# Performance work log

Hardware: AMD Instinct MI355X
Metric: run time of the kernel (lower is better)

Reference implementation:

```python
import jax, jax.numpy as jnp
import numpy as np

B, N = 2, 131072          # batch, expanded node slots (divisible by flag_size)
FEAT = 69                 # org(3) + pos(3) + uids(63)
KERNELS = 128
FLAG_SIZE = 4             # 1 << dims, dims = 2
BINS = 16                 # 1 << flag_size


def _conv1d(x, w, b, stride=1, padding='SAME'):
    # keras Conv1D: x [B,N,Cin], w [K,Cin,Cout], relu activation
    y = jax.lax.conv_general_dilated(x, w, (stride,), padding,
                                     dimension_numbers=('NWC', 'WIO', 'NWC'))
    return jax.nn.relu(y + b)


def setup_inputs() -> dict:
    key = jax.random.key(0)
    ks = jax.random.split(key, 12)

    def g(k, shape):
        fan_in = int(np.prod(shape[:-1]))
        return (jax.random.normal(k, shape, jnp.float32) / np.sqrt(fan_in)).astype(jnp.float32)

    c_x = FEAT + KERNELS                 # 197 after each pre conv concat
    c_flags = 2 * FEAT + KERNELS         # 266 flags-head input
    c_sym = c_flags + FLAG_SIZE          # 270 symbols-branch input

    return {
        'inputs': jax.random.normal(ks[0], (B, N, FEAT), jnp.float32),
        'w_pre0': g(ks[1], (3, FEAT, KERNELS)),   'b_pre0': jnp.zeros((KERNELS,), jnp.float32),
        'w_pre1': g(ks[2], (3, c_x, KERNELS)),    'b_pre1': jnp.zeros((KERNELS,), jnp.float32),
        'w_flags': g(ks[3], (c_flags, FLAG_SIZE)), 'b_flags': jnp.zeros((FLAG_SIZE,), jnp.float32),
        'w_merge': g(ks[4], (FLAG_SIZE, c_sym, KERNELS)), 'b_merge': jnp.zeros((KERNELS,), jnp.float32),
        'w_post0': g(ks[5], (3, KERNELS, KERNELS)), 'b_post0': jnp.zeros((KERNELS,), jnp.float32),
        'w_post1': g(ks[6], (3, KERNELS, KERNELS)), 'b_post1': jnp.zeros((KERNELS,), jnp.float32),
        'w_post2': g(ks[7], (3, KERNELS, KERNELS)), 'b_post2': jnp.zeros((KERNELS,), jnp.float32),
        'w_post3': g(ks[8], (3, KERNELS, KERNELS)), 'b_post3': jnp.zeros((KERNELS,), jnp.float32),
        'w_sym': g(ks[9], (KERNELS, BINS)),        'b_sym': jnp.zeros((BINS,), jnp.float32),
    }


def _forward(inputs, w_pre0, b_pre0, w_pre1, b_pre1, w_flags, b_flags,
             w_merge, b_merge, w_post0, b_post0, w_post1, b_post1,
             w_post2, b_post2, w_post3, b_post3, w_sym, b_sym):
    # pos offsets = (3, 6); pos = inputs[..., 3:5] (2 columns)
    pos = inputs[..., 3:5]
    sort = jnp.argsort(pos, axis=-2)                       # [B, N, 2]
    # gather with batch_dims=1 along node axis
    X = jnp.take_along_axis(inputs, sort[..., 1:2], axis=1)   # sorted by pos col 1
    x0 = jax.lax.stop_gradient(X)                            # [B, N, 69]
    X = jnp.concatenate([x0, _conv1d(X, w_pre0, b_pre0)], axis=-1)  # [B, N, 197]
    X = jnp.concatenate([x0, _conv1d(X, w_pre1, b_pre1)], axis=-1)  # [B, N, 197]
    X = jnp.concatenate([X, jnp.take_along_axis(inputs, sort[..., 0:1], axis=1)], axis=-1)  # [B, N, 266]

    F = jax.nn.sigmoid(X @ w_flags + b_flags)               # [B, N, 4]

    S = jax.lax.stop_gradient(jnp.concatenate([F, X], axis=-1))     # [B, N, 270]
    S = _conv1d(S, w_merge, b_merge, stride=FLAG_SIZE, padding='VALID')  # [B, N/4, 128]
    for w, b in ((w_post0, b_post0), (w_post1, b_post1), (w_post2, b_post2), (w_post3, b_post3)):
        S = _conv1d(S, w, b)
    S = jax.nn.softmax(S @ w_sym + b_sym, axis=-1)          # [B, N/4, 16]

    Fd = (F[..., 0] - F[..., 1]).reshape(F.shape[0], -1, FLAG_SIZE)  # [B, N/4, 4]
    return jnp.concatenate([Fd, S], axis=-1)                # [B, N/4, 20]


def reference(inputs, w_pre0, b_pre0, w_pre1, b_pre1, w_flags, b_flags,
              w_merge, b_merge, w_post0, b_post0, w_post1, b_post1,
              w_post2, b_post2, w_post3, b_post3, w_sym, b_sym):
    return _forward(inputs, w_pre0, b_pre0, w_pre1, b_pre1, w_flags, b_flags,
                    w_merge, b_merge, w_post0, b_post0, w_post1, b_post1,
                    w_post2, b_post2, w_post3, b_post3, w_sym, b_sym)
```

## Files before the change

kernel.cpp:

```cpp
#include <hip/hip_runtime.h>
#include <hip/hip_bf16.h>
#include <math.h>

#define NPOS 131072
#define NF   69
#define NMRG 32768
#define TILE 2048
#define TPS  64
#define NSORT 4

typedef __attribute__((ext_vector_type(8))) short short8;
typedef __bf16 bf16x8 __attribute__((ext_vector_type(8)));
typedef __attribute__((ext_vector_type(4))) float f32x4;

static __device__ inline bf16x8 as_bf16x8(short8 v){ union{short8 s; bf16x8 b;} u; u.s=v; return u.b; }
static __device__ inline short f2bf(float x){ __hip_bfloat16 h = __float2bfloat16(x); return *(short*)&h; }
static __device__ inline float bf2f(short s){ return __uint_as_float(((unsigned)(unsigned short)s)<<16); }

static __device__ inline void gld16(const short* g, short* l){
  __builtin_amdgcn_global_load_lds(
      (const __attribute__((address_space(1))) unsigned int*)g,
      (__attribute__((address_space(3))) unsigned int*)l, 16, 0, 0);
}

__global__ void k_make_keys(const float* __restrict__ inp, unsigned* __restrict__ kA,
                            unsigned* __restrict__ vA){
  unsigned t = blockIdx.x*256u + threadIdx.x;
  unsigned s = t >> 17, i = t & (NPOS-1u);
  unsigned b = s >> 1, ch = 3u + (s & 1u);
  float x = inp[((size_t)b*NPOS + i)*NF + ch];
  unsigned u = __float_as_uint(x);
  u = (u & 0x80000000u) ? ~u : (u | 0x80000000u);
  kA[t] = u; vA[t] = i;
}

__global__ __launch_bounds__(256) void k_hist(const unsigned* __restrict__ src,
                                              unsigned* __restrict__ hist, int shift){
  __shared__ unsigned h[256];
  int tid = threadIdx.x;
  h[tid] = 0u; __syncthreads();
  int s = blockIdx.x / TPS, tile = blockIdx.x % TPS;
  const unsigned* ks = src + (size_t)s*NPOS + (size_t)tile*TILE;
  for (int r = 0; r < TILE/256; ++r){
    unsigned d = (ks[r*256 + tid] >> shift) & 255u;
    atomicAdd(&h[d], 1u);
  }
  __syncthreads();
  hist[s*16384 + tid*TPS + tile] = h[tid];
}

__global__ __launch_bounds__(256) void k_scan(unsigned* __restrict__ hist){
  __shared__ unsigned tot[256];
  int tid = threadIdx.x; int s = blockIdx.x;
  unsigned* g = hist + s*16384;
  unsigned sum = 0;
  for (int q = 0; q < 64; ++q) sum += g[tid*64 + q];
  tot[tid] = sum;
  __syncthreads();
  if (tid == 0){
    unsigned run = 0;
    for (int t = 0; t < 256; ++t){ unsigned tmp = tot[t]; tot[t] = run; run += tmp; }
  }
  __syncthreads();
  unsigned run = tot[tid];
  for (int q = 0; q < 64; ++q){ unsigned tmp = g[tid*64+q]; g[tid*64+q] = run; run += tmp; }
}

#define EPT 16
__global__ __launch_bounds__(128) void k_scatter(const unsigned* __restrict__ srcK,
    const unsigned* __restrict__ srcV, unsigned* __restrict__ dstK, unsigned* __restrict__ dstV,
    const unsigned* __restrict__ off, int shift){
  __shared__ unsigned short cnt[256*128];
  int tid = threadIdx.x;
  unsigned* cz = (unsigned*)cnt;
  for (int idx = tid; idx < 256*128/2; idx += 128) cz[idx] = 0u;
  __syncthreads();
  int s = blockIdx.x / TPS, tile = blockIdx.x % TPS;
  const unsigned* ks = srcK + (size_t)s*NPOS + (size_t)tile*TILE;
  const unsigned* vs = srcV + (size_t)s*NPOS + (size_t)tile*TILE;
  unsigned k8[EPT], v8[EPT];
  #pragma unroll
  for (int r = 0; r < EPT; ++r){
    k8[r] = ks[tid*EPT + r];
    v8[r] = vs[tid*EPT + r];
    unsigned d = (k8[r] >> shift) & 255u;
    cnt[d*128 + tid]++;
  }
  __syncthreads();
  for (int dd = 0; dd < 2; ++dd){
    int d = tid + dd*128;
    unsigned run = 0;
    for (int t = 0; t < 128; ++t){ unsigned tmp = cnt[d*128 + t]; cnt[d*128 + t] = (unsigned short)run; run += tmp; }
  }
  __syncthreads();
  const unsigned* ob = off + s*16384;
  #pragma unroll
  for (int r = 0; r < EPT; ++r){
    unsigned d = (k8[r] >> shift) & 255u;
    unsigned rk = cnt[d*128 + tid];
    cnt[d*128 + tid] = (unsigned short)(rk + 1u);
    unsigned pos = ob[d*TPS + tile] + rk;
    dstK[(size_t)s*NPOS + pos] = k8[r];
    dstV[(size_t)s*NPOS + pos] = v8[r];
  }
}

__global__ __launch_bounds__(256) void k_gath(const float* __restrict__ inp,
    const unsigned* __restrict__ P1, const unsigned* __restrict__ P0,
    short* __restrict__ XA, short* __restrict__ Xcat, int b){
  int t = blockIdx.x*256 + threadIdx.x;
  int i = t >> 7, c = t & 127;
  if (c < 69){
    short s1 = f2bf(inp[((size_t)b*NPOS + P1[i])*NF + c]);
    XA[(size_t)i*224 + 128 + c] = s1;
    Xcat[(size_t)i*272 + 132 + c] = s1;
    Xcat[(size_t)i*272 + 201 + c] = f2bf(inp[((size_t)b*NPOS + P0[i])*NF + c]);
  } else if (c == 69){
    Xcat[(size_t)i*272 + 270] = 0;
    Xcat[(size_t)i*272 + 271] = 0;
  }
}

__global__ void k_prepB(const float* __restrict__ w, short* __restrict__ out,
                        int KC, int NQ, int mode, int total){
  int t = blockIdx.x*256 + threadIdx.x;
  if (t >= total) return;
  int lane = t & 63, ni = (t>>6) & 1, ksub = (t>>7) & 1;
  int rest = t >> 8;
  int q = rest % NQ;
  int wv = rest / NQ;
  int tap = q / KC, cc = q - tap*KC;
  int nn = wv*32 + ni*16 + (lane & 15);
  int chb = cc*64 + ksub*32 + ((lane >> 4) & 3)*8;
  short o[8];
  #pragma unroll
  for (int e = 0; e < 8; ++e){
    int ch = chb + e;
    float val = 0.f;
    if (mode == 0){ if (ch < 69)  val = w[((size_t)tap*69  + ch)*128 + nn]; }
    else if (mode == 1){
      if (ch < 128)      val = w[((size_t)tap*197 + 69 + ch)*128 + nn];
      else if (ch < 197) val = w[((size_t)tap*197 + ch - 128)*128 + nn];
    }
    else if (mode == 2){ if (ch < 128) val = w[((size_t)tap*128 + ch)*128 + nn]; }
    else {
      int tm = ch / 272, cm = ch - tm*272;
      int orig = -1;
      if (cm < 128)      orig = 73 + cm;
      else if (cm < 201) orig = cm - 128;
      else if (cm < 270) orig = cm;
      if (orig >= 0) val = w[((size_t)tm*270 + orig)*128 + nn];
    }
    o[e] = f2bf(val);
  }
  *(short8*)(out + (size_t)t*8) = *(short8*)o;
}

__global__ void k_prepWf(const float* __restrict__ wf, float* __restrict__ out){
  int t = blockIdx.x*256 + threadIdx.x;
  if (t >= 1088) return;
  int c = t >> 2, q = t & 3;
  float v = 0.f;
  if (c < 128)                 v = wf[(69 + c)*4 + q];
  else if (c >= 132 && c < 201) v = wf[(c - 132)*4 + q];
  else if (c >= 201 && c < 270) v = wf[(197 + c - 201)*4 + q];
  out[t] = v;
}

#define OSTR 132

template<int CPAD>
__global__ __launch_bounds__(256) void k_conv3r(
    const short* __restrict__ src, int sstride, int coff, int cin,
    const short* __restrict__ wB, const float* __restrict__ bias,
    short* __restrict__ dst, int dstride, int n)
{
  constexpr int KC = CPAD/64;
  constexpr int NSTEP = 3*KC;
  constexpr int ASTR = CPAD + 8;
  constexpr int AG = CPAD/8;
  constexpr size_t ABYTES = (size_t)66*ASTR*2;
  constexpr size_t OBYTES = (size_t)64*OSTR*4;
  constexpr size_t LBYTES = (ABYTES > OBYTES) ? ABYTES : OBYTES;
  __shared__ __attribute__((aligned(16))) char LDS[LBYTES];
  short* A_s = (short*)LDS;
  float* OT  = (float*)LDS;
  int tid = threadIdx.x;
  int i0 = blockIdx.x*64;
  int wv = tid >> 6, lane = tid & 63;
  int lm = lane & 15, lk = lane >> 4;

  for (int idx = tid; idx < 66*AG; idx += 256){
    int r = idx / AG, g = idx - r*AG;
    int pos = i0 - 1 + r;
    short8 v = {0,0,0,0,0,0,0,0};
    if (pos >= 0 && pos < n && g*8 < cin){
      const short* sp = src + (size_t)pos*sstride + coff + g*8;
      if (g*8 + 8 <= cin) v = *(const short8*)sp;
      else { for (int j = 0; g*8 + j < cin; ++j) v[j] = sp[j]; }
    }
    *(short8*)(A_s + r*ASTR + g*8) = v;
  }
  __syncthreads();

  const short* wBw = wB + (size_t)wv*NSTEP*2048 + (size_t)lane*8;
  f32x4 acc[4][2] = {};
  #pragma unroll
  for (int tp = 0; tp < 3; ++tp){
    bf16x8 bfr[KC][2][2];
    #pragma unroll
    for (int c = 0; c < KC; ++c)
      #pragma unroll
      for (int ksub = 0; ksub < 2; ++ksub)
        #pragma unroll
        for (int ni = 0; ni < 2; ++ni)
          bfr[c][ksub][ni] = as_bf16x8(*(const short8*)(
              wBw + (((size_t)(tp*KC + c)*2 + ksub)*2 + ni)*512));
    #pragma unroll
    for (int c = 0; c < KC; ++c){
      #pragma unroll
      for (int ksub = 0; ksub < 2; ++ksub){
        bf16x8 a[4];
        #pragma unroll
        for (int mi = 0; mi < 4; ++mi)
          a[mi] = as_bf16x8(*(const short8*)(A_s + (mi*16+lm+tp)*ASTR + c*64 + ksub*32 + lk*8));
        #pragma unroll
        for (int mi = 0; mi < 4; ++mi)
          #pragma unroll
          for (int ni = 0; ni < 2; ++ni)
            acc[mi][ni] = __builtin_amdgcn_mfma_f32_16x16x32_bf16(a[mi], bfr[c][ksub][ni], acc[mi][ni], 0, 0, 0);
      }
    }
  }
  __syncthreads();
  float b0 = bias[wv*32 + lm], b1 = bias[wv*32 + 16 + lm];
  #pragma unroll
  for (int mi = 0; mi < 4; ++mi)
    #pragma unroll
    for (int ni = 0; ni < 2; ++ni){
      float bb = ni ? b1 : b0;
      #pragma unroll
      for (int r = 0; r < 4; ++r)
        OT[(mi*16 + lk*4 + r)*OSTR + wv*32 + ni*16 + lm] = fmaxf(acc[mi][ni][r] + bb, 0.f);
    }
  __syncthreads();
  {
    int r = tid >> 2, q = tid & 3;
    const float* row = OT + r*OSTR + q*32;
    short o[32];
    #pragma unroll
    for (int jc = 0; jc < 8; ++jc){
      f32x4 v = *(const f32x4*)(row + jc*4);
      #pragma unroll
      for (int e = 0; e < 4; ++e) o[jc*4+e] = f2bf(v[e]);
    }
    short* dp = dst + (size_t)(i0 + r)*dstride + q*32;
    #pragma unroll
    for (int v8 = 0; v8 < 4; ++v8) *(short8*)(dp + v8*8) = *(short8*)(o + v8*8);
  }
}

__global__ __launch_bounds__(256) void k_mergem3(const short* __restrict__ Xf,
    const short* __restrict__ wB, const float* __restrict__ bias, short* __restrict__ dst)
{
  constexpr size_t OBYTES = (size_t)64*OSTR*4;
  __shared__ __attribute__((aligned(16))) char LDS[OBYTES];
  short* A_s = (short*)LDS;
  float* OT  = (float*)LDS;
  int tid = threadIdx.x;
  int j0 = blockIdx.x*64;
  int wv = tid >> 6, lane = tid & 63;
  int lm = lane & 15, lk = lane >> 4;
  auto stageA = [&](int s){
    #pragma unroll
    for (int it = 0; it < 2; ++it){
      int slot = it*256 + tid;
      int r = slot >> 3, kv = slot & 7;
      const short* gp = Xf + (size_t)(j0 + r)*1088 + s*64 + ((kv ^ (r&7))*8);
      gld16(gp, A_s + (s&1)*4096 + slot*8);
    }
  };
  const short* wBl = wB + (size_t)wv*17*2048 + (size_t)lane*8;
  auto LB = [&](int s, int ks, int ni){
    return as_bf16x8(*(const short8*)(wBl + ((size_t)(s*2 + ks)*2 + ni)*512));
  };
  bf16x8 c00 = LB(0,0,0), c01 = LB(0,0,1), c10 = LB(0,1,0), c11 = LB(0,1,1);
  stageA(0);
  __syncthreads();
  f32x4 acc[4][2] = {};
  for (int s = 0; s < 17; ++s){
    bf16x8 n00, n01, n10, n11;
    if (s < 16){
      n00 = LB(s+1,0,0); n01 = LB(s+1,0,1); n10 = LB(s+1,1,0); n11 = LB(s+1,1,1);
      stageA(s+1);
    }
    const short* Ab = A_s + (s&1)*4096;
    bf16x8 a[4];
    #pragma unroll
    for (int mi = 0; mi < 4; ++mi){
      int r = mi*16 + lm;
      a[mi] = as_bf16x8(*(const short8*)(Ab + r*64 + ((lk ^ (r&7))*8)));
    }
    #pragma unroll
    for (int mi = 0; mi < 4; ++mi){
      acc[mi][0] = __builtin_amdgcn_mfma_f32_16x16x32_bf16(a[mi], c00, acc[mi][0], 0, 0, 0);
      acc[mi][1] = __builtin_amdgcn_mfma_f32_16x16x32_bf16(a[mi], c01, acc[mi][1], 0, 0, 0);
    }
    #pragma unroll
    for (int mi = 0; mi < 4; ++mi){
      int r = mi*16 + lm;
      a[mi] = as_bf16x8(*(const short8*)(Ab + r*64 + (((4+lk) ^ (r&7))*8)));
    }
    #pragma unroll
    for (int mi = 0; mi < 4; ++mi){
      acc[mi][0] = __builtin_amdgcn_mfma_f32_16x16x32_bf16(a[mi], c10, acc[mi][0], 0, 0, 0);
      acc[mi][1] = __builtin_amdgcn_mfma_f32_16x16x32_bf16(a[mi], c11, acc[mi][1], 0, 0, 0);
    }
    __syncthreads();
    c00 = n00; c01 = n01; c10 = n10; c11 = n11;
  }
  float b0 = bias[wv*32 + lm], b1 = bias[wv*32 + 16 + lm];
  #pragma unroll
  for (int mi = 0; mi < 4; ++mi)
    #pragma unroll
    for (int ni = 0; ni < 2; ++ni){
      float bb = ni ? b1 : b0;
      #pragma unroll
      for (int r = 0; r < 4; ++r)
        OT[(mi*16 + lk*4 + r)*OSTR + wv*32 + ni*16 + lm] = fmaxf(acc[mi][ni][r] + bb, 0.f);
    }
  __syncthreads();
  {
    int r = tid >> 2, q = tid & 3;
    const float* row = OT + r*OSTR + q*32;
    short o[32];
    #pragma unroll
    for (int jc = 0; jc < 8; ++jc){
      f32x4 v = *(const f32x4*)(row + jc*4);
      #pragma unroll
      for (int e = 0; e < 4; ++e) o[jc*4+e] = f2bf(v[e]);
    }
    short* dp = dst + (size_t)(j0 + r)*128 + q*32;
    #pragma unroll
    for (int v8 = 0; v8 < 4; ++v8) *(short8*)(dp + v8*8) = *(short8*)(o + v8*8);
  }
}

__global__ __launch_bounds__(256) void k_flags2(short* __restrict__ Xcat,
    const float* __restrict__ Wf2, const float* __restrict__ bf, float* __restrict__ F){
  size_t i = (size_t)blockIdx.x*256 + threadIdx.x;
  const short* x = Xcat + i*272;
  float a0 = bf[0], a1 = bf[1], a2 = bf[2], a3 = bf[3];
  for (int g = 0; g < 34; ++g){
    short8 x8 = *(const short8*)(x + g*8);
    #pragma unroll
    for (int e = 0; e < 8; ++e){
      float xv = bf2f(x8[e]);
      const float* w = Wf2 + (g*8+e)*4;
      a0 = fmaf(xv,w[0],a0); a1 = fmaf(xv,w[1],a1); a2 = fmaf(xv,w[2],a2); a3 = fmaf(xv,w[3],a3);
    }
  }
  float f0 = 1.f/(1.f+expf(-a0)), f1 = 1.f/(1.f+expf(-a1));
  float f2 = 1.f/(1.f+expf(-a2)), f3 = 1.f/(1.f+expf(-a3));
  float* f = F + i*4;
  f[0]=f0; f[1]=f1; f[2]=f2; f[3]=f3;
  short* xc = Xcat + i*272 + 128;
  xc[0]=f2bf(f0); xc[1]=f2bf(f1); xc[2]=f2bf(f2); xc[3]=f2bf(f3);
}

__global__ __launch_bounds__(256) void k_out(const short* __restrict__ S,
    const float* __restrict__ F, const float* __restrict__ Ws, const float* __restrict__ bs,
    float* __restrict__ out, int b){
  size_t j = (size_t)blockIdx.x*256 + threadIdx.x;
  float l[16];
  #pragma unroll
  for (int t = 0; t < 16; ++t) l[t] = bs[t];
  const short* s = S + j*128;
  for (int g = 0; g < 16; ++g){
    short8 x8 = *(const short8*)(s + g*8);
    #pragma unroll
    for (int e = 0; e < 8; ++e){
      float x = bf2f(x8[e]);
      const float* w = Ws + (g*8+e)*16;
      #pragma unroll
      for (int t = 0; t < 16; ++t) l[t] = fmaf(x, w[t], l[t]);
    }
  }
  float m = l[0];
  #pragma unroll
  for (int t = 1; t < 16; ++t) m = fmaxf(m, l[t]);
  float sum = 0.f;
  #pragma unroll
  for (int t = 0; t < 16; ++t){ l[t] = expf(l[t]-m); sum += l[t]; }
  float inv = 1.f/sum;
  float* o = out + ((size_t)b*NMRG + j)*20;
  #pragma unroll
  for (int k = 0; k < 4; ++k){
    size_t r = (size_t)(4*j + k)*4;
    o[k] = F[r] - F[r+1];
  }
  #pragma unroll
  for (int t = 0; t < 16; ++t) o[4+t] = l[t]*inv;
}

extern "C" void kernel_launch(void* const* d_in, const int* in_sizes, int n_in,
                              void* d_out, int out_size, void* d_ws, size_t ws_size,
                              hipStream_t stream){
  const float* inp     = (const float*)d_in[0];
  const float* w_pre0  = (const float*)d_in[1];
  const float* b_pre0  = (const float*)d_in[2];
  const float* w_pre1  = (const float*)d_in[3];
  const float* b_pre1  = (const float*)d_in[4];
  const float* w_flags = (const float*)d_in[5];
  const float* b_flags = (const float*)d_in[6];
  const float* w_merge = (const float*)d_in[7];
  const float* b_merge = (const float*)d_in[8];
  const float* w_post[4] = {(const float*)d_in[9], (const float*)d_in[11],
                            (const float*)d_in[13], (const float*)d_in[15]};
  const float* b_post[4] = {(const float*)d_in[10], (const float*)d_in[12],
                            (const float*)d_in[14], (const float*)d_in[16]};
  const float* w_sym   = (const float*)d_in[17];
  const float* b_sym   = (const float*)d_in[18];
  float* outp = (float*)d_out;

  char* p = (char*)d_ws;
  unsigned* kA = (unsigned*)p; p += (size_t)NSORT*NPOS*4;
  unsigned* vA = (unsigned*)p; p += (size_t)NSORT*NPOS*4;
  unsigned* kB = (unsigned*)p; p += (size_t)NSORT*NPOS*4;
  unsigned* vB = (unsigned*)p; p += (size_t)NSORT*NPOS*4;
  unsigned* hist = (unsigned*)p; p += (size_t)NSORT*16384*4;
  short* XA   = (short*)p; p += (size_t)NPOS*224*2;
  short* Xcat = (short*)p; p += (size_t)NPOS*272*2;
  float* Fbuf = (float*)p; p += (size_t)NPOS*4*4;
  short* M0   = (short*)p; p += (size_t)NMRG*128*2;
  short* M1   = (short*)p; p += (size_t)NMRG*128*2;
  short* wb0  = (short*)p; p += (size_t)3*2*8192*2;
  short* wb1  = (short*)p; p += (size_t)3*4*8192*2;
  short* wbq0 = (short*)p; p += (size_t)3*2*8192*2;
  short* wbq1 = (short*)p; p += (size_t)3*2*8192*2;
  short* wbq2 = (short*)p; p += (size_t)3*2*8192*2;
  short* wbq3 = (short*)p; p += (size_t)3*2*8192*2;
  short* wbm  = (short*)p; p += (size_t)17*8192*2;
  float* wf2  = (float*)p; p += (size_t)272*4*4;
  if ((size_t)(p - (char*)d_ws) > ws_size) return;
  short* wbq[4] = {wbq0, wbq1, wbq2, wbq3};

  k_prepB<<<(6144 +255)/256, 256, 0, stream>>>(w_pre0, wb0, 2, 6, 0, 6144);
  k_prepB<<<(12288+255)/256, 256, 0, stream>>>(w_pre1, wb1, 4, 12, 1, 12288);
  for (int i = 0; i < 4; ++i)
    k_prepB<<<(6144+255)/256, 256, 0, stream>>>(w_post[i], wbq[i], 2, 6, 2, 6144);
  k_prepB<<<(17408+255)/256, 256, 0, stream>>>(w_merge, wbm, 17, 17, 3, 17408);
  k_prepWf<<<5, 256, 0, stream>>>(w_flags, wf2);

  k_make_keys<<<NSORT*NPOS/256, 256, 0, stream>>>(inp, kA, vA);
  unsigned *sk = kA, *sv = vA, *dk = kB, *dv = vB;
  for (int pass = 0; pass < 4; ++pass){
    int shift = pass*8;
    k_hist<<<NSORT*TPS, 256, 0, stream>>>(sk, hist, shift);
    k_scan<<<NSORT, 256, 0, stream>>>(hist);
    k_scatter<<<NSORT*TPS, 128, 0, stream>>>(sk, sv, dk, dv, hist, shift);
    unsigned* t;
    t = sk; sk = dk; dk = t;
    t = sv; sv = dv; dv = t;
  }
  for (int b = 0; b < 2; ++b){
    const unsigned* P0 = sv + (size_t)(b*2+0)*NPOS;
    const unsigned* P1 = sv + (size_t)(b*2+1)*NPOS;
    k_gath<<<NPOS*128/256, 256, 0, stream>>>(inp, P1, P0, XA, Xcat, b);
    k_conv3r<128><<<NPOS/64, 256, 0, stream>>>(XA, 224, 128, 69,  wb0, b_pre0, XA,   224, NPOS);
    k_conv3r<256><<<NPOS/64, 256, 0, stream>>>(XA, 224, 0,   197, wb1, b_pre1, Xcat, 272, NPOS);
    k_flags2<<<NPOS/256, 256, 0, stream>>>(Xcat, wf2, b_flags, Fbuf);
    k_mergem3<<<NMRG/64, 256, 0, stream>>>(Xcat, wbm, b_merge, M0);
    k_conv3r<128><<<NMRG/64, 256, 0, stream>>>(M0, 128, 0, 128, wbq[0], b_post[0], M1, 128, NMRG);
    k_conv3r<128><<<NMRG/64, 256, 0, stream>>>(M1, 128, 0, 128, wbq[1], b_post[1], M0, 128, NMRG);
    k_conv3r<128><<<NMRG/64, 256, 0, stream>>>(M0, 128, 0, 128, wbq[2], b_post[2], M1, 128, NMRG);
    k_conv3r<128><<<NMRG/64, 256, 0, stream>>>(M1, 128, 0, 128, wbq[3], b_post[3], M0, 128, NMRG);
    k_out<<<NMRG/256, 256, 0, stream>>>(M0, Fbuf, w_sym, b_sym, outp, b);
  }
}
```

Before: 596.5 us.

## Shrink radix-sort tiles for more blocks and prefetch conv weights in a ring

The radix sort now uses 512-element tiles with 256 tiles per sort, 64-thread scatter blocks and a padded per-digit count stride. This gives more blocks and a smaller LDS footprint per block, which should raise occupancy. The conv kernel now loads its weight fragments through a 4-deep register prefetch ring overlapped with the A-tile staging, instead of loading each tap's weights all at once. Costs are a larger histogram, a longer serial scan in k_scan, and changed register pressure in the conv.

```diff
diff --git a/kernel.cpp b/kernel.cpp
--- a/kernel.cpp
+++ b/kernel.cpp
@@ -5,9 +5,11 @@
 #define NPOS 131072
 #define NF   69
 #define NMRG 32768
-#define TILE 2048
-#define TPS  64
+#define TILE 512
+#define TPS  256
 #define NSORT 4
+#define EPT  8
+#define CSTR 66
 
 typedef __attribute__((ext_vector_type(8))) short short8;
 typedef __bf16 bf16x8 __attribute__((ext_vector_type(8)));
@@ -39,22 +41,23 @@
   __shared__ unsigned h[256];
   int tid = threadIdx.x;
   h[tid] = 0u; __syncthreads();
-  int s = blockIdx.x / TPS, tile = blockIdx.x % TPS;
+  int s = blockIdx.x >> 8, tile = blockIdx.x & 255;
   const unsigned* ks = src + (size_t)s*NPOS + (size_t)tile*TILE;
+  #pragma unroll
   for (int r = 0; r < TILE/256; ++r){
     unsigned d = (ks[r*256 + tid] >> shift) & 255u;
     atomicAdd(&h[d], 1u);
   }
   __syncthreads();
-  hist[s*16384 + tid*TPS + tile] = h[tid];
+  hist[s*65536 + tid*TPS + tile] = h[tid];
 }
 
 __global__ __launch_bounds__(256) void k_scan(unsigned* __restrict__ hist){
   __shared__ unsigned tot[256];
   int tid = threadIdx.x; int s = blockIdx.x;
-  unsigned* g = hist + s*16384;
+  unsigned* g = hist + s*65536;
   unsigned sum = 0;
-  for (int q = 0; q < 64; ++q) sum += g[tid*64 + q];
+  for (int q = 0; q < TPS; ++q) sum += g[tid*TPS + q];
   tot[tid] = sum;
   __syncthreads();
   if (tid == 0){
@@ -63,19 +66,19 @@
   }
   __syncthreads();
   unsigned run = tot[tid];
-  for (int q = 0; q < 64; ++q){ unsigned tmp = g[tid*64+q]; g[tid*64+q] = run; run += tmp; }
-}
-
-#define EPT 16
-__global__ __launch_bounds__(128) void k_scatter(const unsigned* __restrict__ srcK,
+  for (int q = 0; q < TPS; ++q){ unsigned tmp = g[tid*TPS+q]; g[tid*TPS+q] = run; run += tmp; }
+}
+
+__global__ __launch_bounds__(64) void k_scatter(const unsigned* __restrict__ srcK,
     const unsigned* __restrict__ srcV, unsigned* __restrict__ dstK, unsigned* __restrict__ dstV,
     const unsigned* __restrict__ off, int shift){
-  __shared__ unsigned short cnt[256*128];
+  __shared__ unsigned short cnt[256*CSTR];
   int tid = threadIdx.x;
-  unsigned* cz = (unsigned*)cnt;
-  for (int idx = tid; idx < 256*128/2; idx += 128) cz[idx] = 0u;
-  __syncthreads();
-  int s = blockIdx.x / TPS, tile = blockIdx.x % TPS;
+  short8* cz = (short8*)cnt;
+  short8 z = {0,0,0,0,0,0,0,0};
+  for (int idx = tid; idx < 256*CSTR/8; idx += 64) cz[idx] = z;
+  __syncthreads();
+  int s = blockIdx.x >> 8, tile = blockIdx.x & 255;
   const unsigned* ks = srcK + (size_t)s*NPOS + (size_t)tile*TILE;
   const unsigned* vs = srcV + (size_t)s*NPOS + (size_t)tile*TILE;
   unsigned k8[EPT], v8[EPT];
@@ -84,21 +87,22 @@
     k8[r] = ks[tid*EPT + r];
     v8[r] = vs[tid*EPT + r];
     unsigned d = (k8[r] >> shift) & 255u;
-    cnt[d*128 + tid]++;
-  }
-  __syncthreads();
-  for (int dd = 0; dd < 2; ++dd){
-    int d = tid + dd*128;
+    cnt[d*CSTR + tid]++;
+  }
+  __syncthreads();
+  #pragma unroll
+  for (int dd = 0; dd < 4; ++dd){
+    int d = tid + dd*64;
     unsigned run = 0;
-    for (int t = 0; t < 128; ++t){ unsigned tmp = cnt[d*128 + t]; cnt[d*128 + t] = (unsigned short)run; run += tmp; }
-  }
-  __syncthreads();
-  const unsigned* ob = off + s*16384;
+    for (int t = 0; t < 64; ++t){ unsigned tmp = cnt[d*CSTR + t]; cnt[d*CSTR + t] = (unsigned short)run; run += tmp; }
+  }
+  __syncthreads();
+  const unsigned* ob = off + s*65536;
   #pragma unroll
   for (int r = 0; r < EPT; ++r){
     unsigned d = (k8[r] >> shift) & 255u;
-    unsigned rk = cnt[d*128 + tid];
-    cnt[d*128 + tid] = (unsigned short)(rk + 1u);
+    unsigned rk = cnt[d*CSTR + tid];
+    cnt[d*CSTR + tid] = (unsigned short)(rk + 1u);
     unsigned pos = ob[d*TPS + tile] + rk;
     dstK[(size_t)s*NPOS + pos] = k8[r];
     dstV[(size_t)s*NPOS + pos] = v8[r];
@@ -170,13 +174,14 @@
 #define OSTR 132
 
 template<int CPAD>
-__global__ __launch_bounds__(256) void k_conv3r(
+__global__ __launch_bounds__(256) void k_conv3p(
     const short* __restrict__ src, int sstride, int coff, int cin,
     const short* __restrict__ wB, const float* __restrict__ bias,
     short* __restrict__ dst, int dstride, int n)
 {
   constexpr int KC = CPAD/64;
-  constexpr int NSTEP = 3*KC;
+  constexpr int NSTEP2 = 3*KC*2;
+  constexpr int PF = 4;
   constexpr int ASTR = CPAD + 8;
   constexpr int AG = CPAD/8;
   constexpr size_t ABYTES = (size_t)66*ASTR*2;
@@ -190,6 +195,14 @@
   int wv = tid >> 6, lane = tid & 63;
   int lm = lane & 15, lk = lane >> 4;
 
+  const short* wBw = wB + (size_t)wv*NSTEP2*1024 + (size_t)lane*8;
+  auto LB = [&](int ss, int ni){
+    return as_bf16x8(*(const short8*)(wBw + (ss*2 + ni)*512));
+  };
+  bf16x8 bq[PF][2];
+  #pragma unroll
+  for (int s = 0; s < PF; ++s){ bq[s][0] = LB(s,0); bq[s][1] = LB(s,1); }
+
   for (int idx = tid; idx < 66*AG; idx += 256){
     int r = idx / AG, g = idx - r*AG;
     int pos = i0 - 1 + r;
@@ -203,42 +216,31 @@
   }
   __syncthreads();
 
-  const short* wBw = wB + (size_t)wv*NSTEP*2048 + (size_t)lane*8;
   f32x4 acc[4][2] = {};
   #pragma unroll
-  for (int tp = 0; tp < 3; ++tp){
-    bf16x8 bfr[KC][2][2];
-    #pragma unroll
-    for (int c = 0; c < KC; ++c)
-      #pragma unroll
-      for (int ksub = 0; ksub < 2; ++ksub)
-        #pragma unroll
-        for (int ni = 0; ni < 2; ++ni)
-          bfr[c][ksub][ni] = as_bf16x8(*(const short8*)(
-              wBw + (((size_t)(tp*KC + c)*2 + ksub)*2 + ni)*512));
-    #pragma unroll
-    for (int c = 0; c < KC; ++c){
-      #pragma unroll
-      for (int ksub = 0; ksub < 2; ++ksub){
-        bf16x8 a[4];
-        #pragma unroll
-        for (int mi = 0; mi < 4; ++mi)
-          a[mi] = as_bf16x8(*(const short8*)(A_s + (mi*16+lm+tp)*ASTR + c*64 + ksub*32 + lk*8));
-        #pragma unroll
-        for (int mi = 0; mi < 4; ++mi)
-          #pragma unroll
-          for (int ni = 0; ni < 2; ++ni)
-            acc[mi][ni] = __builtin_amdgcn_mfma_f32_16x16x32_bf16(a[mi], bfr[c][ksub][ni], acc[mi][ni], 0, 0, 0);
-      }
-    }
-  }
-  __syncthreads();
-  float b0 = bias[wv*32 + lm], b1 = bias[wv*32 + 16 + lm];
+  for (int ss = 0; ss < NSTEP2; ++ss){
+    int slot = ss % PF;
+    bf16x8 b0 = bq[slot][0], b1 = bq[slot][1];
+    if (ss + PF < NSTEP2){ bq[slot][0] = LB(ss+PF,0); bq[slot][1] = LB(ss+PF,1); }
+    int q = ss >> 1, ksub = ss & 1;
+    int tp = q / KC, c = q - tp*KC;
+    bf16x8 a[4];
+    #pragma unroll
+    for (int mi = 0; mi < 4; ++mi)
+      a[mi] = as_bf16x8(*(const short8*)(A_s + (mi*16+lm+tp)*ASTR + c*64 + ksub*32 + lk*8));
+    #pragma unroll
+    for (int mi = 0; mi < 4; ++mi){
+      acc[mi][0] = __builtin_amdgcn_mfma_f32_16x16x32_bf16(a[mi], b0, acc[mi][0], 0, 0, 0);
+      acc[mi][1] = __builtin_amdgcn_mfma_f32_16x16x32_bf16(a[mi], b1, acc[mi][1], 0, 0, 0);
+    }
+  }
+  __syncthreads();
+  float b0s = bias[wv*32 + lm], b1s = bias[wv*32 + 16 + lm];
   #pragma unroll
   for (int mi = 0; mi < 4; ++mi)
     #pragma unroll
     for (int ni = 0; ni < 2; ++ni){
-      float bb = ni ? b1 : b0;
+      float bb = ni ? b1s : b0s;
       #pragma unroll
       for (int r = 0; r < 4; ++r)
         OT[(mi*16 + lk*4 + r)*OSTR + wv*32 + ni*16 + lm] = fmaxf(acc[mi][ni][r] + bb, 0.f);
@@ -428,7 +430,7 @@
   unsigned* vA = (unsigned*)p; p += (size_t)NSORT*NPOS*4;
   unsigned* kB = (unsigned*)p; p += (size_t)NSORT*NPOS*4;
   unsigned* vB = (unsigned*)p; p += (size_t)NSORT*NPOS*4;
-  unsigned* hist = (unsigned*)p; p += (size_t)NSORT*16384*4;
+  unsigned* hist = (unsigned*)p; p += (size_t)NSORT*65536*4;
   short* XA   = (short*)p; p += (size_t)NPOS*224*2;
   short* Xcat = (short*)p; p += (size_t)NPOS*272*2;
   float* Fbuf = (float*)p; p += (size_t)NPOS*4*4;
@@ -458,7 +460,7 @@
     int shift = pass*8;
     k_hist<<<NSORT*TPS, 256, 0, stream>>>(sk, hist, shift);
     k_scan<<<NSORT, 256, 0, stream>>>(hist);
-    k_scatter<<<NSORT*TPS, 128, 0, stream>>>(sk, sv, dk, dv, hist, shift);
+    k_scatter<<<NSORT*TPS, 64, 0, stream>>>(sk, sv, dk, dv, hist, shift);
     unsigned* t;
     t = sk; sk = dk; dk = t;
     t = sv; sv = dv; dv = t;
@@ -467,14 +469,14 @@
     const unsigned* P0 = sv + (size_t)(b*2+0)*NPOS;
     const unsigned* P1 = sv + (size_t)(b*2+1)*NPOS;
     k_gath<<<NPOS*128/256, 256, 0, stream>>>(inp, P1, P0, XA, Xcat, b);
-    k_conv3r<128><<<NPOS/64, 256, 0, stream>>>(XA, 224, 128, 69,  wb0, b_pre0, XA,   224, NPOS);
-    k_conv3r<256><<<NPOS/64, 256, 0, stream>>>(XA, 224, 0,   197, wb1, b_pre1, Xcat, 272, NPOS);
+    k_conv3p<128><<<NPOS/64, 256, 0, stream>>>(XA, 224, 128, 69,  wb0, b_pre0, XA,   224, NPOS);
+    k_conv3p<256><<<NPOS/64, 256, 0, stream>>>(XA, 224, 0,   197, wb1, b_pre1, Xcat, 272, NPOS);
     k_flags2<<<NPOS/256, 256, 0, stream>>>(Xcat, wf2, b_flags, Fbuf);
     k_mergem3<<<NMRG/64, 256, 0, stream>>>(Xcat, wbm, b_merge, M0);
-    k_conv3r<128><<<NMRG/64, 256, 0, stream>>>(M0, 128, 0, 128, wbq[0], b_post[0], M1, 128, NMRG);
-    k_conv3r<128><<<NMRG/64, 256, 0, stream>>>(M1, 128, 0, 128, wbq[1], b_post[1], M0, 128, NMRG);
-    k_conv3r<128><<<NMRG/64, 256, 0, stream>>>(M0, 128, 0, 128, wbq[2], b_post[2], M1, 128, NMRG);
-    k_conv3r<128><<<NMRG/64, 256, 0, stream>>>(M1, 128, 0, 128, wbq[3], b_post[3], M0, 128, NMRG);
+    k_conv3p<128><<<NMRG/64, 256, 0, stream>>>(M0, 128, 0, 128, wbq[0], b_post[0], M1, 128, NMRG);
+    k_conv3p<128><<<NMRG/64, 256, 0, stream>>>(M1, 128, 0, 128, wbq[1], b_post[1], M0, 128, NMRG);
+    k_conv3p<128><<<NMRG/64, 256, 0, stream>>>(M0, 128, 0, 128, wbq[2], b_post[2], M1, 128, NMRG);
+    k_conv3p<128><<<NMRG/64, 256, 0, stream>>>(M1, 128, 0, 128, wbq[3], b_post[3], M0, 128, NMRG);
     k_out<<<NMRG/256, 256, 0, stream>>>(M0, Fbuf, w_sym, b_sym, outp, b);
   }
 }
```

Result: slower. 640.3 us (+7.3%).
